# Kernel tuning notes

Measured on AMD Instinct MI355X. Metric: run time of the kernel, lower is better.

## Reference

```python
import jax, jax.numpy as jnp
import numpy as np

N_FEATURE = 40
EMBED_DIM = 64
HIDDEN = 64
OUT_DIM = 1
BATCH = 2048

# pairwise indices (i<j), fixed constants
_ROW, _COL = np.triu_indices(N_FEATURE, k=1)
ROW = jnp.asarray(_ROW)
COL = jnp.asarray(_COL)


def setup_inputs() -> dict:
    key = jax.random.key(0)
    ks = jax.random.split(key, 7)
    s_e = 1.0 / np.sqrt(EMBED_DIM)
    s_h = 1.0 / np.sqrt(HIDDEN)
    return {
        "x": jax.random.normal(ks[0], (BATCH, N_FEATURE, EMBED_DIM), jnp.float32),
        "W1": jax.random.uniform(ks[1], (HIDDEN, EMBED_DIM), jnp.float32, -s_e, s_e),
        "b1": jax.random.uniform(ks[2], (HIDDEN,), jnp.float32, -s_e, s_e),
        "W2": jax.random.uniform(ks[3], (1, HIDDEN), jnp.float32, -s_h, s_h),
        "b2": jax.random.uniform(ks[4], (1,), jnp.float32, -s_h, s_h),
        "Wl": jax.random.uniform(ks[5], (OUT_DIM, EMBED_DIM), jnp.float32, -s_e, s_e),
        "bl": jax.random.uniform(ks[6], (OUT_DIM,), jnp.float32, -s_e, s_e),
    }


def reference(x, W1, b1, W2, b2, Wl, bl):
    # pairwise elementwise products: [B, P, E]
    p = x[:, ROW, :]
    q = x[:, COL, :]
    inner = p * q
    # small attention MLP: Linear -> ReLU -> Linear -> softmax over pairs dim
    h = jax.nn.relu(jnp.einsum('bpe,he->bph', inner, W1) + b1)
    logits = jnp.einsum('bph,oh->bpo', h, W2) + b2  # [B, P, 1]
    attn = jax.nn.softmax(logits, axis=1)
    # softmax-weighted sum over pairs -> [B, E]
    pooled = jnp.sum(inner * attn, axis=1)
    # final linear (dropout p=0 is identity)
    return pooled @ Wl.T + bl
```

## Files before the change

### kernel.cpp

```cpp
#include <hip/hip_runtime.h>
#include <math.h>

#define NF 40
#define ED 64
#define NP 780
#define BT 256
#define NT 13

typedef __attribute__((ext_vector_type(8))) _Float16 f16x8;
typedef __attribute__((ext_vector_type(2))) __fp16  fp16x2;
typedef __attribute__((ext_vector_type(4))) float   f32x4;

__global__ __launch_bounds__(BT, 4)
void afm_mfma16f_kernel(const float* __restrict__ x,
                        const float* __restrict__ W1,
                        const float* __restrict__ b1,
                        const float* __restrict__ W2,
                        const float* __restrict__ Wl,
                        const float* __restrict__ blp,
                        float* __restrict__ out)
{
    __shared__ __align__(16) unsigned char sxh[NF * 128];
    __shared__ __align__(16) unsigned char sfrag[10 * 64 * 16];
    __shared__ unsigned short srct[NP];
    __shared__ float srede[4], sreds[4];

    const int b    = blockIdx.x;
    const int tid  = threadIdx.x;
    const int lane = tid & 63;
    const int w    = tid >> 6;
    const int ln15 = lane & 15;
    const int g    = lane >> 4;

    {
        const float4* xg = (const float4*)(x + (size_t)b * NF * ED);
        for (int u = tid; u < NF * 16; u += BT) {
            float4 v = xg[u];
            const int r = u >> 4, j = u & 15;
            union { fp16x2 h2[2]; unsigned long long ll; } pk;
            pk.h2[0] = __builtin_amdgcn_cvt_pkrtz(v.x, v.y);
            pk.h2[1] = __builtin_amdgcn_cvt_pkrtz(v.z, v.w);
            const int byteoff = r * 128 + (((j >> 1) ^ (r & 7)) << 4) + (j & 1) * 8;
            *(unsigned long long*)(sxh + byteoff) = pk.ll;
        }
        if (tid < 64) {
            #pragma unroll
            for (int f = 0; f < 10; ++f) {
                const float* src = (f < 8)
                    ? (W1 + ((f >> 1) * 16 + ln15) * ED + (f & 1) * 32 + g * 8)
                    : (Wl + (f - 8) * 32 + g * 8);
                union { fp16x2 h2[4]; f16x8 h8; } u;
                u.h2[0] = __builtin_amdgcn_cvt_pkrtz(src[0], src[1]);
                u.h2[1] = __builtin_amdgcn_cvt_pkrtz(src[2], src[3]);
                u.h2[2] = __builtin_amdgcn_cvt_pkrtz(src[4], src[5]);
                u.h2[3] = __builtin_amdgcn_cvt_pkrtz(src[6], src[7]);
                *(f16x8*)(sfrag + (f * 64 + tid) * 16) = u.h8;
            }
        }
        for (int p = tid; p < NP; p += BT) {
            const int r = (int)((79.0f - sqrtf(6241.0f - 8.0f * (float)p)) * 0.5f);
            const int c = p - ((r * (79 - r)) >> 1) + r + 1;
            srct[p] = (unsigned short)(r | (c << 8));
        }
    }

    f32x4  b1v[4];
    fp16x2 w2h[4][2];
    #pragma unroll
    for (int mf = 0; mf < 4; ++mf) {
        float4 wv = *(const float4*)(W2 + mf * 16 + g * 4);
        b1v[mf] = *(const f32x4*)(b1 + mf * 16 + g * 4);
        w2h[mf][0] = __builtin_amdgcn_cvt_pkrtz(wv.x, wv.y);
        w2h[mf][1] = __builtin_amdgcn_cvt_pkrtz(wv.z, wv.w);
    }

    __syncthreads();

    f16x8 Ah[4][2], Awl[2];
    #pragma unroll
    for (int mf = 0; mf < 4; ++mf)
        #pragma unroll
        for (int ks = 0; ks < 2; ++ks)
            Ah[mf][ks] = *(const f16x8*)(sfrag + ((mf * 2 + ks) * 64 + lane) * 16);
    #pragma unroll
    for (int ks = 0; ks < 2; ++ks)
        Awl[ks] = *(const f16x8*)(sfrag + ((8 + ks) * 64 + lane) * 16);

    const f32x4 zero4 = {0.f, 0.f, 0.f, 0.f};
    const fp16x2 zh = {(__fp16)0.f, (__fp16)0.f};

    float le = 0.f, les = 0.f;
    for (int tile = 0; tile < NT; ++tile) {
        const int p  = tile * 64 + w * 16 + ln15;
        const int pc = p < NP ? p : NP - 1;
        const unsigned int rc = srct[pc];
        const int r = rc & 255, c = rc >> 8;

        f16x8 Bf[2];
        #pragma unroll
        for (int ks = 0; ks < 2; ++ks) {
            const int s16 = ks * 4 + g;
            f16x8 xr = *(const f16x8*)(sxh + r * 128 + ((s16 ^ (r & 7)) << 4));
            f16x8 xc = *(const f16x8*)(sxh + c * 128 + ((s16 ^ (c & 7)) << 4));
            Bf[ks] = xr * xc;
        }

        f32x4 sacc;
        sacc = __builtin_amdgcn_mfma_f32_16x16x32_f16(Awl[0], Bf[0], zero4, 0, 0, 0);
        sacc = __builtin_amdgcn_mfma_f32_16x16x32_f16(Awl[1], Bf[1], sacc, 0, 0, 0);

        f32x4 acc[4];
        #pragma unroll
        for (int mf = 0; mf < 4; ++mf) {
            acc[mf] = __builtin_amdgcn_mfma_f32_16x16x32_f16(Ah[mf][0], Bf[0], b1v[mf], 0, 0, 0);
            acc[mf] = __builtin_amdgcn_mfma_f32_16x16x32_f16(Ah[mf][1], Bf[1], acc[mf], 0, 0, 0);
        }

        float q0 = 0.f, q1 = 0.f;
        #pragma unroll
        for (int mf = 0; mf < 4; ++mf) {
            fp16x2 h01 = __builtin_amdgcn_cvt_pkrtz(acc[mf][0], acc[mf][1]);
            fp16x2 h23 = __builtin_amdgcn_cvt_pkrtz(acc[mf][2], acc[mf][3]);
            h01 = __builtin_elementwise_max(h01, zh);
            h23 = __builtin_elementwise_max(h23, zh);
            if (mf & 1) {
                q1 = __builtin_amdgcn_fdot2(h01, w2h[mf][0], q1, false);
                q1 = __builtin_amdgcn_fdot2(h23, w2h[mf][1], q1, false);
            } else {
                q0 = __builtin_amdgcn_fdot2(h01, w2h[mf][0], q0, false);
                q0 = __builtin_amdgcn_fdot2(h23, w2h[mf][1], q0, false);
            }
        }
        float part = q0 + q1;
        part += __shfl_xor(part, 16);
        part += __shfl_xor(part, 32);

        const float e_ = (p < NP) ? __expf(part) : 0.f;
        le  += e_;
        les  = fmaf(e_, sacc[0], les);
    }

    #pragma unroll
    for (int off = 1; off < 16; off <<= 1) {
        le  += __shfl_xor(le, off);
        les += __shfl_xor(les, off);
    }
    if (lane == 0) { srede[w] = le; sreds[w] = les; }
    __syncthreads();

    if (tid == 0) {
        float E  = srede[0] + srede[1] + srede[2] + srede[3];
        float ES = sreds[0] + sreds[1] + sreds[2] + sreds[3];
        out[b] = ES / E + blp[0];
    }
}

extern "C" void kernel_launch(void* const* d_in, const int* in_sizes, int n_in,
                              void* d_out, int out_size, void* d_ws, size_t ws_size,
                              hipStream_t stream) {
    const float* x  = (const float*)d_in[0];
    const float* W1 = (const float*)d_in[1];
    const float* b1 = (const float*)d_in[2];
    const float* W2 = (const float*)d_in[3];
    const float* Wl = (const float*)d_in[5];
    const float* bl = (const float*)d_in[6];
    float* out = (float*)d_out;

    const int B = in_sizes[0] / (NF * ED);
    afm_mfma16f_kernel<<<B, BT, 0, stream>>>(x, W1, b1, W2, Wl, bl, out);
}
```

Measured before the change: 29.86 us.

## Map one batch row per wavefront and pack eight rows per block

Each wavefront now handles one whole batch row, iterating over all 49 padded 16-pair tiles itself. Blocks become 512 threads covering eight rows, so the weight-fragment conversion and pair-index table setup are shared across eight rows. The cross-wave shared-memory reduction and the final __syncthreads are dropped, since each wave writes its own output. In exchange the grid shrinks to B/8 blocks with fewer resident waves per CU, which can reduce latency hiding, and it assumes the batch is divisible by eight.

```diff
diff --git a/kernel.cpp b/kernel.cpp
--- a/kernel.cpp
+++ b/kernel.cpp
@@ -4,15 +4,16 @@
 #define NF 40
 #define ED 64
 #define NP 780
-#define BT 256
-#define NT 13
+#define GPB 8
+#define BT 512
+#define NT 49
 
 typedef __attribute__((ext_vector_type(8))) _Float16 f16x8;
 typedef __attribute__((ext_vector_type(2))) __fp16  fp16x2;
 typedef __attribute__((ext_vector_type(4))) float   f32x4;
 
-__global__ __launch_bounds__(BT, 4)
-void afm_mfma16f_kernel(const float* __restrict__ x,
+__global__ __launch_bounds__(BT, 2)
+void afm_mfma16g_kernel(const float* __restrict__ x,
                         const float* __restrict__ W1,
                         const float* __restrict__ b1,
                         const float* __restrict__ W2,
@@ -20,48 +21,52 @@
                         const float* __restrict__ blp,
                         float* __restrict__ out)
 {
-    __shared__ __align__(16) unsigned char sxh[NF * 128];
+    __shared__ __align__(16) unsigned char sxh[GPB * NF * 128];
     __shared__ __align__(16) unsigned char sfrag[10 * 64 * 16];
-    __shared__ unsigned short srct[NP];
-    __shared__ float srede[4], sreds[4];
+    __shared__ unsigned short srct[784];
 
-    const int b    = blockIdx.x;
     const int tid  = threadIdx.x;
     const int lane = tid & 63;
     const int w    = tid >> 6;
     const int ln15 = lane & 15;
     const int g    = lane >> 4;
 
+    const int b0 = blockIdx.x * GPB + w;
+    unsigned char* sxw = sxh + w * (NF * 128);
+
     {
-        const float4* xg = (const float4*)(x + (size_t)b * NF * ED);
-        for (int u = tid; u < NF * 16; u += BT) {
+        const float4* xg = (const float4*)(x + (size_t)b0 * NF * ED);
+        #pragma unroll
+        for (int i = 0; i < 10; ++i) {
+            const int u = lane + i * 64;
             float4 v = xg[u];
             const int r = u >> 4, j = u & 15;
             union { fp16x2 h2[2]; unsigned long long ll; } pk;
             pk.h2[0] = __builtin_amdgcn_cvt_pkrtz(v.x, v.y);
             pk.h2[1] = __builtin_amdgcn_cvt_pkrtz(v.z, v.w);
             const int byteoff = r * 128 + (((j >> 1) ^ (r & 7)) << 4) + (j & 1) * 8;
-            *(unsigned long long*)(sxh + byteoff) = pk.ll;
+            *(unsigned long long*)(sxw + byteoff) = pk.ll;
         }
-        if (tid < 64) {
-            #pragma unroll
-            for (int f = 0; f < 10; ++f) {
-                const float* src = (f < 8)
-                    ? (W1 + ((f >> 1) * 16 + ln15) * ED + (f & 1) * 32 + g * 8)
-                    : (Wl + (f - 8) * 32 + g * 8);
-                union { fp16x2 h2[4]; f16x8 h8; } u;
-                u.h2[0] = __builtin_amdgcn_cvt_pkrtz(src[0], src[1]);
-                u.h2[1] = __builtin_amdgcn_cvt_pkrtz(src[2], src[3]);
-                u.h2[2] = __builtin_amdgcn_cvt_pkrtz(src[4], src[5]);
-                u.h2[3] = __builtin_amdgcn_cvt_pkrtz(src[6], src[7]);
-                *(f16x8*)(sfrag + (f * 64 + tid) * 16) = u.h8;
-            }
-        }
-        for (int p = tid; p < NP; p += BT) {
-            const int r = (int)((79.0f - sqrtf(6241.0f - 8.0f * (float)p)) * 0.5f);
-            const int c = p - ((r * (79 - r)) >> 1) + r + 1;
-            srct[p] = (unsigned short)(r | (c << 8));
-        }
+    }
+
+    for (int slot = tid; slot < 640; slot += BT) {
+        const int f = slot >> 6, l = slot & 63;
+        const int lg = l >> 4, l15 = l & 15;
+        const float* src = (f < 8)
+            ? (W1 + ((f >> 1) * 16 + l15) * ED + (f & 1) * 32 + lg * 8)
+            : (Wl + (f - 8) * 32 + lg * 8);
+        union { fp16x2 h2[4]; f16x8 h8; } u;
+        u.h2[0] = __builtin_amdgcn_cvt_pkrtz(src[0], src[1]);
+        u.h2[1] = __builtin_amdgcn_cvt_pkrtz(src[2], src[3]);
+        u.h2[2] = __builtin_amdgcn_cvt_pkrtz(src[4], src[5]);
+        u.h2[3] = __builtin_amdgcn_cvt_pkrtz(src[6], src[7]);
+        *(f16x8*)(sfrag + slot * 16) = u.h8;
+    }
+    for (int p = tid; p < 784; p += BT) {
+        const int pq = p < NP ? p : NP - 1;
+        const int r = (int)((79.0f - sqrtf(6241.0f - 8.0f * (float)pq)) * 0.5f);
+        const int c = pq - ((r * (79 - r)) >> 1) + r + 1;
+        srct[p] = (unsigned short)(r | (c << 8));
     }
 
     f32x4  b1v[4];
@@ -73,6 +78,7 @@
         w2h[mf][0] = __builtin_amdgcn_cvt_pkrtz(wv.x, wv.y);
         w2h[mf][1] = __builtin_amdgcn_cvt_pkrtz(wv.z, wv.w);
     }
+    const float blv = blp[0];
 
     __syncthreads();
 
@@ -91,17 +97,16 @@
 
     float le = 0.f, les = 0.f;
     for (int tile = 0; tile < NT; ++tile) {
-        const int p  = tile * 64 + w * 16 + ln15;
-        const int pc = p < NP ? p : NP - 1;
-        const unsigned int rc = srct[pc];
+        const int p = tile * 16 + ln15;
+        const unsigned int rc = srct[p];
         const int r = rc & 255, c = rc >> 8;
 
         f16x8 Bf[2];
         #pragma unroll
         for (int ks = 0; ks < 2; ++ks) {
             const int s16 = ks * 4 + g;
-            f16x8 xr = *(const f16x8*)(sxh + r * 128 + ((s16 ^ (r & 7)) << 4));
-            f16x8 xc = *(const f16x8*)(sxh + c * 128 + ((s16 ^ (c & 7)) << 4));
+            f16x8 xr = *(const f16x8*)(sxw + r * 128 + ((s16 ^ (r & 7)) << 4));
+            f16x8 xc = *(const f16x8*)(sxw + c * 128 + ((s16 ^ (c & 7)) << 4));
             Bf[ks] = xr * xc;
         }
 
@@ -145,14 +150,7 @@
         le  += __shfl_xor(le, off);
         les += __shfl_xor(les, off);
     }
-    if (lane == 0) { srede[w] = le; sreds[w] = les; }
-    __syncthreads();
-
-    if (tid == 0) {
-        float E  = srede[0] + srede[1] + srede[2] + srede[3];
-        float ES = sreds[0] + sreds[1] + sreds[2] + sreds[3];
-        out[b] = ES / E + blp[0];
-    }
+    if (lane == 0) out[b0] = les / le + blv;
 }
 
 extern "C" void kernel_launch(void* const* d_in, const int* in_sizes, int n_in,
@@ -167,5 +165,5 @@
     float* out = (float*)d_out;
 
     const int B = in_sizes[0] / (NF * ED);
-    afm_mfma16f_kernel<<<B, BT, 0, stream>>>(x, W1, b1, W2, Wl, bl, out);
+    afm_mfma16g_kernel<<<B / GPB, BT, 0, stream>>>(x, W1, b1, W2, Wl, bl, out);
 }
```

Result: faster. 27.67 us (-7.3%).
